# Kernel optimization log

Measured on AMD Instinct MI355X. Metric: run time of the kernel, lower is better.

Reference implementation:

```python
import jax, jax.numpy as jnp
import numpy as np

WS = 2048            # window_size
STEP = WS // 2       # hop = window_size // 2
NC = WS // 2 + 1     # rfft coeffs
NB = 4               # n_blocks


def _hann():
    # periodic hann window (torch.hann_window default)
    return 0.5 - 0.5 * jnp.cos(2.0 * jnp.pi * jnp.arange(WS) / WS)


def _block(x, transfer, gain):
    # x: (b, 1, time); transfer: (NC,); gain: scalar
    b, ch, time = x.shape
    frames = time // STEP
    padded = jnp.pad(x, ((0, 0), (0, 0), (0, STEP)))
    idx = jnp.arange(frames)[:, None] * STEP + jnp.arange(WS)[None, :]
    windowed = padded[:, :, idx]                       # (b, ch, F, WS)
    spec = jnp.fft.rfft(windowed, axis=-1)             # (b, ch, F, NC) complex
    spec_t = jnp.moveaxis(spec, 2, 0)                  # (F, b, ch, NC)
    tc = transfer.astype(spec.dtype)

    # linear recurrence: out_i = transfer * (spec_i + out_{i-1})
    def step_fn(carry, s):
        out = (s + carry) * tc
        return out, out

    _, outs = jax.lax.scan(step_fn, jnp.zeros_like(spec_t[0]), spec_t)
    wins = jnp.fft.irfft(outs, n=WS, axis=-1) * _hann()  # (F, b, ch, WS)
    wins = jnp.moveaxis(wins, 0, 2)                      # (b, ch, F, WS)
    # overlap-add with hop = WS/2: split each frame into two halves
    first = wins[..., :STEP].reshape(b, ch, frames * STEP)
    second = wins[..., STEP:].reshape(b, ch, frames * STEP)
    samples = (jnp.pad(first, ((0, 0), (0, 0), (0, STEP)))
               + jnp.pad(second, ((0, 0), (0, 0), (STEP, 0))))
    return jnp.tanh(samples * gain)[..., :time]


def setup_inputs() -> dict:
    key = jax.random.key(0)
    k_x, k_b, k_s, k_g = jax.random.split(key, 4)
    x = jax.random.normal(k_x, (32, 1, 262144), dtype=jnp.float32)
    # init_transfer: sparse resonances * scaling * pitch^2
    resonances = (jax.random.uniform(k_b, (NB, NC)) < 0.01).astype(jnp.float32)
    scaling = jax.random.uniform(k_s, (NB, NC), minval=0.9, maxval=0.998)
    pitch = jnp.linspace(1.0, 0.0, NC) ** 2
    transfers = resonances * scaling * pitch[None, :]
    gains = jax.random.uniform(k_g, (NB,), minval=10.0, maxval=200.0)
    mixer = jnp.zeros((NB + 1,), dtype=jnp.float32)
    return {"x": x, "transfers": transfers, "gains": gains, "mixer": mixer}


def reference(x, transfers, gains, mixer):
    outputs = [x]
    inp = x
    for i in range(NB):
        inp = _block(inp, transfers[i], gains[i])
        outputs.append(inp)
    stacked = jnp.stack(outputs, axis=-1)          # (b, 1, time, NB+1)
    mixer_values = jax.nn.softmax(mixer)
    return jnp.sum(stacked * mixer_values, axis=-1)
```

## Files before the change

kernel.cpp:

```cpp
#include <hip/hip_runtime.h>
#include <math.h>
#include <stdint.h>

#define NB   4
#define NC   1025
#define WSZ  2048
#define STEP 1024
#define FRM  256
#define BAT  32
#define TT   262144
#define SEGS 4
#define KC   16
#define YPAD 68

#define RREV (1.0f / 2048.0f)

typedef float f2 __attribute__((ext_vector_type(2)));

__device__ __forceinline__ float tanh_fast(float z) {
    float e = __expf(2.0f * z);
    return 1.0f - 2.0f / (e + 1.0f);
}

__device__ __forceinline__ void cis_rev(int idx, float* c, float* s) {
    float rev = (float)(idx & 2047) * RREV;
    *c = __builtin_amdgcn_cosf(rev);
    *s = __builtin_amdgcn_sinf(rev);
}

__global__ __launch_bounds__(1024) void setup_kernel(
    const float* __restrict__ transfers, const float* __restrict__ mixer,
    int* __restrict__ counts, int* __restrict__ bins, float* __restrict__ tvals,
    float* __restrict__ wmix, float* __restrict__ hann, int kmax)
{
    int i = blockIdx.x, tid = threadIdx.x;
    __shared__ int wcnt[16], woff[16];
    if (i == 0) {
        float cc, ss; cis_rev(tid, &cc, &ss);
        hann[tid] = 0.5f - 0.5f * cc;
    }
    float tv = transfers[i * NC + tid];
    bool nz = (tv != 0.0f);
    unsigned long long mask = __ballot(nz);
    int lane = tid & 63, w = tid >> 6;
    int within = __popcll(mask & ((1ULL << lane) - 1ULL));
    if (lane == 0) wcnt[w] = __popcll(mask);
    __syncthreads();
    if (tid == 0) {
        int acc = 0;
        for (int q = 0; q < 16; ++q) { woff[q] = acc; acc += wcnt[q]; }
        float tvL = transfers[i * NC + 1024];
        if (tvL != 0.0f && acc < kmax) { bins[i * NC + acc] = 1024; tvals[i * NC + acc] = tvL; acc++; }
        counts[i] = (acc < kmax) ? acc : kmax;
        if (i == 0) {
            float m = mixer[0];
            for (int q = 1; q < 5; ++q) m = fmaxf(m, mixer[q]);
            float e[5], s = 0.f;
            for (int q = 0; q < 5; ++q) { e[q] = __expf(mixer[q] - m); s += e[q]; }
            for (int q = 0; q < 5; ++q) wmix[q] = e[q] / s;
        }
    }
    __syncthreads();
    if (nz) {
        int pos = woff[w] + within;
        if (pos < kmax) { bins[i * NC + pos] = tid; tvals[i * NC + pos] = tv; }
    }
}

__global__ __launch_bounds__(256) void table_kernel(
    const int* __restrict__ counts, const int* __restrict__ bins,
    float2* __restrict__ cisA, float2* __restrict__ cisB, int kmax)
{
    int i = blockIdx.x >> 2, c = blockIdx.x & 3;
    int K = counts[i];
    int tid = threadIdx.x;
    for (int j = c; j < K; j += 4) {
        int k = bins[i * NC + j];
        if (tid < 64) {
            float cc, ss; cis_rev(k * tid, &cc, &ss);
            cisA[((size_t)i * kmax + j) * 64 + tid] = make_float2(cc, ss);
        } else if (tid < 80) {
            int q = tid - 64;
            float cc, ss; cis_rev(k * 64 * q, &cc, &ss);
            cisB[((size_t)i * kmax + j) * 16 + q] = make_float2(cc, ss);
        }
    }
}

__device__ __forceinline__ void half_dft(
    const float xr[16], int K, const float2* __restrict__ cA,
    const float2* __restrict__ cB, float2* __restrict__ Hout, int lane, int w)
{
    for (int j = w; j < K; j += 8) {
        int j2 = j + 4;
        bool two = (j2 < K);
        float2 bA = cB[(size_t)j * 16 + 1];
        float2 bB = two ? cB[(size_t)j2 * 16 + 1] : bA;
        float2 wAl = cA[(size_t)j * 64 + lane];
        float2 wBl = two ? cA[(size_t)j2 * 64 + lane] : wAl;
        f2 Wr, Wi, nWi;
        Wr.x = bA.x; Wr.y = bB.x;
        Wi.x = -bA.y; Wi.y = -bB.y;
        nWi = -Wi;
        f2 hr = 0.f, hi = 0.f;
#pragma unroll
        for (int i = 15; i >= 0; --i) {
            f2 xx; xx.x = xr[i]; xx.y = xr[i];
            f2 tmp = nWi * hi + xx;
            f2 nr = Wr * hr + tmp;
            hi = Wi * hr + Wr * hi;
            hr = nr;
        }
        f2 wlc, wls;
        wlc.x = wAl.x; wlc.y = wBl.x;
        wls.x = wAl.y; wls.y = wBl.y;
        f2 re = hr * wlc + hi * wls;
        f2 im = hi * wlc - hr * wls;
        float reA = re.x, imA = im.x, reB = re.y, imB = im.y;
#pragma unroll
        for (int m = 32; m >= 1; m >>= 1) {
            reA += __shfl_xor(reA, m, 64);
            imA += __shfl_xor(imA, m, 64);
            reB += __shfl_xor(reB, m, 64);
            imB += __shfl_xor(imB, m, 64);
        }
        if (lane == 0) {
            Hout[j] = make_float2(reA, imA);
            if (two) Hout[j2] = make_float2(reB, imB);
        }
    }
}

__global__ __launch_bounds__(256, 8) void analysis_kernel(
    const float* __restrict__ x, const int* __restrict__ counts,
    const float2* __restrict__ cisA, const float2* __restrict__ cisB,
    float2* __restrict__ H, int iblk, int kmax)
{
    int wg = blockIdx.x;
    int b = wg >> 8, h = wg & 255;
    int tid = threadIdx.x;
    int lane = tid & 63, w = tid >> 6;
    int K = counts[iblk];
    const float* xb = x + (size_t)b * TT + (size_t)h * STEP;
    float xr[16];
#pragma unroll
    for (int i = 0; i < 16; ++i) xr[i] = xb[lane + (i << 6)];
    const float2* cA = cisA + (size_t)iblk * kmax * 64;
    const float2* cB = cisB + (size_t)iblk * kmax * 16;
    float2* Hout = H + (size_t)(b * FRM + h) * K;
    half_dft(xr, K, cA, cB, Hout, lane, w);
}

__global__ __launch_bounds__(256) void scan_kernel(
    float2* __restrict__ S, const int* __restrict__ counts,
    const int* __restrict__ bins, const float* __restrict__ tvals, int iblk)
{
    int K = counts[iblk];
    int gw = (blockIdx.x << 2) + (threadIdx.x >> 6);
    int lane = threadIdx.x & 63;
    int b = gw & (BAT - 1), j0 = gw >> 5;
    for (int j = j0; j < K; j += 32) {
        float t = tvals[iblk * NC + j];
        int k = bins[iblk * NC + j];
        float sgn = (k & 1) ? -t : t;
        float2* Sb = S + (size_t)b * FRM * K + j;
        int f0 = lane << 2;
        float2 h1_0 = Sb[(size_t)(f0 + 0) * K];
        float2 h1_1 = Sb[(size_t)(f0 + 1) * K];
        float2 h1_2 = Sb[(size_t)(f0 + 2) * K];
        float2 h1_3 = Sb[(size_t)(f0 + 3) * K];
        float2 h1_4 = (f0 + 4 < FRM) ? Sb[(size_t)(f0 + 4) * K] : make_float2(0.f, 0.f);
        float ax0 = fmaf(sgn, h1_1.x, h1_0.x * t), ay0 = fmaf(sgn, h1_1.y, h1_0.y * t);
        float ax1 = fmaf(sgn, h1_2.x, h1_1.x * t), ay1 = fmaf(sgn, h1_2.y, h1_1.y * t);
        float ax2 = fmaf(sgn, h1_3.x, h1_2.x * t), ay2 = fmaf(sgn, h1_3.y, h1_2.y * t);
        float ax3 = fmaf(sgn, h1_4.x, h1_3.x * t), ay3 = fmaf(sgn, h1_4.y, h1_3.y * t);
        float Ax0 = ax0,                  Ay0 = ay0;
        float Ax1 = fmaf(t, Ax0, ax1),    Ay1 = fmaf(t, Ay0, ay1);
        float Ax2 = fmaf(t, Ax1, ax2),    Ay2 = fmaf(t, Ay1, ay2);
        float Ax3 = fmaf(t, Ax2, ax3),    Ay3 = fmaf(t, Ay2, ay3);
        float t2 = t * t, t4 = t2 * t2;
        float Px = Ax3, Py = Ay3;
        float w = t4;
#pragma unroll
        for (int d = 1; d <= 32; d <<= 1) {
            float ux = __shfl_up(Px, d, 64);
            float uy = __shfl_up(Py, d, 64);
            if (lane >= d) { Px = fmaf(w, ux, Px); Py = fmaf(w, uy, Py); }
            w *= w;
        }
        float Cx = __shfl_up(Px, 1, 64);
        float Cy = __shfl_up(Py, 1, 64);
        if (lane == 0) { Cx = 0.f; Cy = 0.f; }
        float t3 = t2 * t;
        Sb[(size_t)(f0 + 0) * K] = make_float2(fmaf(t,  Cx, Ax0), fmaf(t,  Cy, Ay0));
        Sb[(size_t)(f0 + 1) * K] = make_float2(fmaf(t2, Cx, Ax1), fmaf(t2, Cy, Ay1));
        Sb[(size_t)(f0 + 2) * K] = make_float2(fmaf(t3, Cx, Ax2), fmaf(t3, Cy, Ay2));
        Sb[(size_t)(f0 + 3) * K] = make_float2(fmaf(t4, Cx, Ax3), fmaf(t4, Cy, Ay3));
    }
}

__device__ __forceinline__ void acc4(
    f2& q0, f2& q1, f2& q2, f2& q3, float4 e, float4 a0, float4 a1)
{
    f2 up; up.x = e.x; up.y = e.y;
    f2 vp; vp.x = e.z; vp.y = e.w;
    q0 = up * a0.x + q0; q0 = vp * a0.y + q0;
    q1 = up * a0.z + q1; q1 = vp * a0.w + q1;
    q2 = up * a1.x + q2; q2 = vp * a1.y + q2;
    q3 = up * a1.z + q3; q3 = vp * a1.w + q3;
}

__global__ __launch_bounds__(256, 5) void fused_synth_kernel(
    const float2* __restrict__ S, float2* __restrict__ H2,
    const float2* __restrict__ cisA, const float2* __restrict__ cisB,
    const int* __restrict__ counts, const int* __restrict__ bins,
    const float* __restrict__ gains, const float* __restrict__ wmix,
    const float* __restrict__ hann, const float* __restrict__ x,
    float* __restrict__ dout, int iblk, int do_an, int kmax)
{
    __shared__ float4 smem[1216];
    float4* rc = smem;
    float*  ystage = (float*)smem;
    float4* part = smem + 1088;

    int wg = blockIdx.x;
    int b = wg >> 6, s0 = (wg & 63) << 2;
    int tid = threadIdx.x;
    int n1 = tid << 2;
    int q = tid >> 4;
    int m = (tid & 15) << 2;

    int K = counts[iblk];
    const int* bl = bins + iblk * NC;
    const float2* Ob = S + (size_t)b * FRM * K;
    const float2* cA0 = cisA + (size_t)iblk * kmax * 64;
    const float2* cB0 = cisB + (size_t)iblk * kmax * 16;

    f2 p00 = 0.f, p01 = 0.f, p02 = 0.f, p03 = 0.f;
    f2 p10 = 0.f, p11 = 0.f, p12 = 0.f, p13 = 0.f;
    f2 p20 = 0.f, p21 = 0.f, p22 = 0.f, p23 = 0.f;
    f2 p30 = 0.f, p31 = 0.f, p32 = 0.f, p33 = 0.f;

    for (int c0 = 0; c0 < K; c0 += KC) {
        int cs = (K - c0 < KC) ? (K - c0) : KC;
        {
            int flat = tid >> 2;
            int seg = flat >> 4;
            int j = flat & 15;
            int jj = c0 + ((j < cs) ? j : (cs - 1));
            int q0 = (tid & 3) << 2;
            int k = bl[jj];
            float g = ((k == 0) || (k == 1024)) ? (1.0f / 2048.0f) : (2.0f / 2048.0f);
            float sg = (k & 1) ? -g : g;
            int fc = s0 + seg;
            float2 o1 = Ob[(size_t)fc * K + jj];
            float2 om = (fc > 0) ? Ob[(size_t)(fc - 1) * K + jj] : make_float2(0.f, 0.f);
            float c2r = om.x * sg, c2i = om.y * sg;
            f2 u; u.x = c2r;  u.y = o1.x * g - c2r;
            f2 v; v.x = -c2i; v.y = -(o1.y * g - c2i);
            const float2* bqp = cB0 + (size_t)jj * 16 + q0;
#pragma unroll
            for (int e = 0; e < 4; ++e) {
                float2 bq = bqp[e];
                f2 up = u * bq.x + v * bq.y;
                f2 vp = v * bq.x - u * bq.y;
                rc[(flat << 4) + q0 + e] = make_float4(up.x, up.y, vp.x, vp.y);
            }
        }
        __syncthreads();
        const float2* cAj = cA0 + ((size_t)c0 << 6) + m;
        const float4* rcq = rc + q;
        int jj = 0;
        for (; jj + 2 <= cs; jj += 2) {
            float4 a00 = *(const float4*)(cAj);
            float4 a01 = *(const float4*)(cAj + 2);
            float4 a10 = *(const float4*)(cAj + 64);
            float4 a11 = *(const float4*)(cAj + 66);
            cAj += 128;
            {
                float4 e0 = rcq[(0 * KC + jj) << 4];
                float4 e1 = rcq[(0 * KC + jj + 1) << 4];
                acc4(p00, p01, p02, p03, e0, a00, a01);
                acc4(p00, p01, p02, p03, e1, a10, a11);
            }
            {
                float4 e0 = rcq[(1 * KC + jj) << 4];
                float4 e1 = rcq[(1 * KC + jj + 1) << 4];
                acc4(p10, p11, p12, p13, e0, a00, a01);
                acc4(p10, p11, p12, p13, e1, a10, a11);
            }
            {
                float4 e0 = rcq[(2 * KC + jj) << 4];
                float4 e1 = rcq[(2 * KC + jj + 1) << 4];
                acc4(p20, p21, p22, p23, e0, a00, a01);
                acc4(p20, p21, p22, p23, e1, a10, a11);
            }
            {
                float4 e0 = rcq[(3 * KC + jj) << 4];
                float4 e1 = rcq[(3 * KC + jj + 1) << 4];
                acc4(p30, p31, p32, p33, e0, a00, a01);
                acc4(p30, p31, p32, p33, e1, a10, a11);
            }
        }
        if (jj < cs) {
            float4 a0 = *(const float4*)(cAj);
            float4 a1 = *(const float4*)(cAj + 2);
            float4 e0 = rcq[(0 * KC + jj) << 4];
            float4 e1 = rcq[(1 * KC + jj) << 4];
            float4 e2 = rcq[(2 * KC + jj) << 4];
            float4 e3 = rcq[(3 * KC + jj) << 4];
            acc4(p00, p01, p02, p03, e0, a0, a1);
            acc4(p10, p11, p12, p13, e1, a0, a1);
            acc4(p20, p21, p22, p23, e2, a0, a1);
            acc4(p30, p31, p32, p33, e3, a0, a1);
        }
        __syncthreads();
    }

    size_t base0 = (size_t)b * TT + ((size_t)s0 << 10) + (size_t)n1;
    const float* prevsrc = (iblk == 0) ? x : dout;
    float4 hv = *(const float4*)(hann + n1);
    float gain = gains[iblk];
    float wsel = (iblk == 0) ? wmix[0] : 1.0f;
    float wn = wmix[iblk + 1];
    int cw = n1 >> 6, off = n1 & 63;

#define SEG_EPI(s, A0, A1, A2, A3)                                              \
    {                                                                           \
        float4 pv = *(const float4*)(prevsrc + base0 + ((size_t)(s) << 10));    \
        float4 yv;                                                              \
        yv.x = tanh_fast(fmaf(hv.x, A0.y, A0.x) * gain);                        \
        yv.y = tanh_fast(fmaf(hv.y, A1.y, A1.x) * gain);                        \
        yv.z = tanh_fast(fmaf(hv.z, A2.y, A2.x) * gain);                        \
        yv.w = tanh_fast(fmaf(hv.w, A3.y, A3.x) * gain);                        \
        float4 dv;                                                              \
        dv.x = fmaf(wsel, pv.x, wn * yv.x);                                     \
        dv.y = fmaf(wsel, pv.y, wn * yv.y);                                     \
        dv.z = fmaf(wsel, pv.z, wn * yv.z);                                     \
        dv.w = fmaf(wsel, pv.w, wn * yv.w);                                     \
        *(float4*)(dout + base0 + ((size_t)(s) << 10)) = dv;                    \
        if (do_an) *(float4*)(ystage + (s) * 16 * YPAD + cw * YPAD + off) = yv; \
    }

    SEG_EPI(0, p00, p01, p02, p03)
    SEG_EPI(1, p10, p11, p12, p13)
    SEG_EPI(2, p20, p21, p22, p23)
    SEG_EPI(3, p30, p31, p32, p33)
#undef SEG_EPI

    if (do_an) {
        __syncthreads();
        int K2 = counts[iblk + 1];
        if (K2 > 0) {
            const float2* cA2 = cisA + (size_t)(iblk + 1) * kmax * 64;
            const float2* cB2 = cisB + (size_t)(iblk + 1) * kmax * 16;
            int jloc = tid & 15, c = tid >> 4;
            int lane = tid & 63, wv = tid >> 6;
            const float4* yp0 = (const float4*)(ystage + c * YPAD);
            const float4* yp1 = (const float4*)(ystage + 16 * YPAD + c * YPAD);
            const float4* yp2 = (const float4*)(ystage + 32 * YPAD + c * YPAD);
            const float4* yp3 = (const float4*)(ystage + 48 * YPAD + c * YPAD);
            for (int jb = 0; jb < K2; jb += 16) {
                int j = jb + jloc;
                int js = (j < K2) ? j : (K2 - 1);
                float2 w1 = cA2[(size_t)js * 64 + 1];
                float Wr = w1.x, Wi = -w1.y, nWi = w1.y;
                f2 hrA = 0.f, hiA = 0.f;
                f2 hrB = 0.f, hiB = 0.f;
#pragma unroll
                for (int i4 = 15; i4 >= 0; --i4) {
                    float4 ya = yp0[i4];
                    float4 yb = yp1[i4];
                    float4 yc = yp2[i4];
                    float4 yd = yp3[i4];
#define HSTEP(CC)                                                                   \
                    { f2 yy; yy.x = ya.CC; yy.y = yb.CC;                            \
                      f2 t = hiA * nWi + yy; f2 nr = hrA * Wr + t;                  \
                      hiA = hrA * Wi + hiA * Wr; hrA = nr; }                        \
                    { f2 yy; yy.x = yc.CC; yy.y = yd.CC;                            \
                      f2 t = hiB * nWi + yy; f2 nr = hrB * Wr + t;                  \
                      hiB = hrB * Wi + hiB * Wr; hrB = nr; }
                    HSTEP(w)
                    HSTEP(z)
                    HSTEP(y)
                    HSTEP(x)
#undef HSTEP
                }
                float2 bq = cB2[(size_t)js * 16 + c];
                f2 reA = hrA * bq.x + hiA * bq.y;
                f2 imA = hiA * bq.x - hrA * bq.y;
                f2 reB = hrB * bq.x + hiB * bq.y;
                f2 imB = hiB * bq.x - hrB * bq.y;
                float4 prA = make_float4(reA.x, imA.x, reA.y, imA.y);
                float4 prB = make_float4(reB.x, imB.x, reB.y, imB.y);
#pragma unroll
                for (int d = 16; d <= 32; d <<= 1) {
                    prA.x += __shfl_xor(prA.x, d, 64);
                    prA.y += __shfl_xor(prA.y, d, 64);
                    prA.z += __shfl_xor(prA.z, d, 64);
                    prA.w += __shfl_xor(prA.w, d, 64);
                    prB.x += __shfl_xor(prB.x, d, 64);
                    prB.y += __shfl_xor(prB.y, d, 64);
                    prB.z += __shfl_xor(prB.z, d, 64);
                    prB.w += __shfl_xor(prB.w, d, 64);
                }
                if (lane < 16) {
                    part[wv * 16 + lane] = prA;
                    part[64 + wv * 16 + lane] = prB;
                }
                __syncthreads();
                if (tid < 32) {
                    int sel = tid >> 4, t = tid & 15;
                    int j2 = jb + t;
                    if (j2 < K2) {
                        const float4* pp = part + sel * 64;
                        float4 a0 = pp[t];
                        float4 a1 = pp[16 + t];
                        float4 a2 = pp[32 + t];
                        float4 a3 = pp[48 + t];
                        float4 acc;
                        acc.x = (a0.x + a1.x) + (a2.x + a3.x);
                        acc.y = (a0.y + a1.y) + (a2.y + a3.y);
                        acc.z = (a0.z + a1.z) + (a2.z + a3.z);
                        acc.w = (a0.w + a1.w) + (a2.w + a3.w);
                        H2[(size_t)(b * FRM + s0 + sel * 2) * K2 + j2] = make_float2(acc.x, acc.y);
                        H2[(size_t)(b * FRM + s0 + sel * 2 + 1) * K2 + j2] = make_float2(acc.z, acc.w);
                    }
                }
                __syncthreads();
            }
        }
    }
}

extern "C" void kernel_launch(void* const* d_in, const int* in_sizes, int n_in,
                              void* d_out, int out_size, void* d_ws, size_t ws_size,
                              hipStream_t stream)
{
    const float* x         = (const float*)d_in[0];
    const float* transfers = (const float*)d_in[1];
    const float* gains     = (const float*)d_in[2];
    const float* mixer     = (const float*)d_in[3];
    float* dout = (float*)d_out;

    uint8_t* ws = (uint8_t*)d_ws;
    int*   counts = (int*)ws;
    int*   bins   = (int*)(ws + 64);
    float* tvals  = (float*)(ws + 64 + 16400);
    float* wmix   = (float*)(ws + 64 + 16400 + 16400);
    float* hann   = (float*)(ws + 36864);
    const size_t HDR = 65536;

    long long perk = 2LL * BAT * FRM * 8 + (long long)NB * 80 * 8;
    long long km = ((long long)ws_size - (long long)HDR) / perk;
    int kmax = (int)((km < 1) ? 1 : ((km > NC) ? NC : km));
    float2* S0 = (float2*)(ws + HDR);
    float2* S1 = S0 + (size_t)BAT * FRM * kmax;
    float2* cisA = S1 + (size_t)BAT * FRM * kmax;
    float2* cisB = cisA + (size_t)NB * kmax * 64;

    setup_kernel<<<NB, 1024, 0, stream>>>(transfers, mixer, counts, bins, tvals, wmix, hann, kmax);
    table_kernel<<<NB * 4, 256, 0, stream>>>(counts, bins, cisA, cisB, kmax);
    analysis_kernel<<<BAT * FRM, 256, 0, stream>>>(x, counts, cisA, cisB, S0, 0, kmax);

    float2* cur = S0;
    float2* nxt = S1;
    for (int i = 0; i < NB; ++i) {
        scan_kernel<<<BAT * 8, 256, 0, stream>>>(cur, counts, bins, tvals, i);
        fused_synth_kernel<<<BAT * (FRM / SEGS), 256, 0, stream>>>(cur, nxt, cisA, cisB, counts, bins,
                                                                   gains, wmix, hann, x, dout, i,
                                                                   (i < NB - 1) ? 1 : 0, kmax);
        float2* t = cur; cur = nxt; nxt = t;
    }
}
```

Before: 235.9 us.

## Fuse recurrence scan into synthesis kernel and fold table build into setup

The separate scan kernel is removed. Each synthesis workgroup now recomputes the per-bin linear recurrence with a wavefront shuffle scan over frames up to its own segment, then stages only the few frames it needs in shared memory via readlane. The cis-table construction is also folded into the setup kernel. Together these drop several kernel launches and a global read-modify-write of the spectrum per block. The cost is redundant scan work in every workgroup, about half the frames on average, plus extra shared-memory syncs per chunk.

```diff
diff --git a/kernel.cpp b/kernel.cpp
--- a/kernel.cpp
+++ b/kernel.cpp
@@ -28,13 +28,19 @@
     *s = __builtin_amdgcn_sinf(rev);
 }
 
+__device__ __forceinline__ float rl(float v, int l) {
+    return __int_as_float(__builtin_amdgcn_readlane(__float_as_int(v), l));
+}
+
 __global__ __launch_bounds__(1024) void setup_kernel(
     const float* __restrict__ transfers, const float* __restrict__ mixer,
     int* __restrict__ counts, int* __restrict__ bins, float* __restrict__ tvals,
-    float* __restrict__ wmix, float* __restrict__ hann, int kmax)
+    float* __restrict__ wmix, float* __restrict__ hann,
+    float2* __restrict__ cisA, float2* __restrict__ cisB, int kmax)
 {
     int i = blockIdx.x, tid = threadIdx.x;
     __shared__ int wcnt[16], woff[16];
+    __shared__ int sK;
     if (i == 0) {
         float cc, ss; cis_rev(tid, &cc, &ss);
         hann[tid] = 0.5f - 0.5f * cc;
@@ -51,7 +57,9 @@
         for (int q = 0; q < 16; ++q) { woff[q] = acc; acc += wcnt[q]; }
         float tvL = transfers[i * NC + 1024];
         if (tvL != 0.0f && acc < kmax) { bins[i * NC + acc] = 1024; tvals[i * NC + acc] = tvL; acc++; }
-        counts[i] = (acc < kmax) ? acc : kmax;
+        int kk = (acc < kmax) ? acc : kmax;
+        counts[i] = kk;
+        sK = kk;
         if (i == 0) {
             float m = mixer[0];
             for (int q = 1; q < 5; ++q) m = fmaxf(m, mixer[q]);
@@ -65,22 +73,16 @@
         int pos = woff[w] + within;
         if (pos < kmax) { bins[i * NC + pos] = tid; tvals[i * NC + pos] = tv; }
     }
-}
-
-__global__ __launch_bounds__(256) void table_kernel(
-    const int* __restrict__ counts, const int* __restrict__ bins,
-    float2* __restrict__ cisA, float2* __restrict__ cisB, int kmax)
-{
-    int i = blockIdx.x >> 2, c = blockIdx.x & 3;
-    int K = counts[i];
-    int tid = threadIdx.x;
-    for (int j = c; j < K; j += 4) {
+    __syncthreads();
+    int K = sK;
+    for (int flat = tid; flat < K * 80; flat += 1024) {
+        int j = flat / 80, r = flat - j * 80;
         int k = bins[i * NC + j];
-        if (tid < 64) {
-            float cc, ss; cis_rev(k * tid, &cc, &ss);
-            cisA[((size_t)i * kmax + j) * 64 + tid] = make_float2(cc, ss);
-        } else if (tid < 80) {
-            int q = tid - 64;
+        if (r < 64) {
+            float cc, ss; cis_rev(k * r, &cc, &ss);
+            cisA[((size_t)i * kmax + j) * 64 + r] = make_float2(cc, ss);
+        } else {
+            int q = r - 64;
             float cc, ss; cis_rev(k * 64 * q, &cc, &ss);
             cisB[((size_t)i * kmax + j) * 16 + q] = make_float2(cc, ss);
         }
@@ -151,54 +153,6 @@
     half_dft(xr, K, cA, cB, Hout, lane, w);
 }
 
-__global__ __launch_bounds__(256) void scan_kernel(
-    float2* __restrict__ S, const int* __restrict__ counts,
-    const int* __restrict__ bins, const float* __restrict__ tvals, int iblk)
-{
-    int K = counts[iblk];
-    int gw = (blockIdx.x << 2) + (threadIdx.x >> 6);
-    int lane = threadIdx.x & 63;
-    int b = gw & (BAT - 1), j0 = gw >> 5;
-    for (int j = j0; j < K; j += 32) {
-        float t = tvals[iblk * NC + j];
-        int k = bins[iblk * NC + j];
-        float sgn = (k & 1) ? -t : t;
-        float2* Sb = S + (size_t)b * FRM * K + j;
-        int f0 = lane << 2;
-        float2 h1_0 = Sb[(size_t)(f0 + 0) * K];
-        float2 h1_1 = Sb[(size_t)(f0 + 1) * K];
-        float2 h1_2 = Sb[(size_t)(f0 + 2) * K];
-        float2 h1_3 = Sb[(size_t)(f0 + 3) * K];
-        float2 h1_4 = (f0 + 4 < FRM) ? Sb[(size_t)(f0 + 4) * K] : make_float2(0.f, 0.f);
-        float ax0 = fmaf(sgn, h1_1.x, h1_0.x * t), ay0 = fmaf(sgn, h1_1.y, h1_0.y * t);
-        float ax1 = fmaf(sgn, h1_2.x, h1_1.x * t), ay1 = fmaf(sgn, h1_2.y, h1_1.y * t);
-        float ax2 = fmaf(sgn, h1_3.x, h1_2.x * t), ay2 = fmaf(sgn, h1_3.y, h1_2.y * t);
-        float ax3 = fmaf(sgn, h1_4.x, h1_3.x * t), ay3 = fmaf(sgn, h1_4.y, h1_3.y * t);
-        float Ax0 = ax0,                  Ay0 = ay0;
-        float Ax1 = fmaf(t, Ax0, ax1),    Ay1 = fmaf(t, Ay0, ay1);
-        float Ax2 = fmaf(t, Ax1, ax2),    Ay2 = fmaf(t, Ay1, ay2);
-        float Ax3 = fmaf(t, Ax2, ax3),    Ay3 = fmaf(t, Ay2, ay3);
-        float t2 = t * t, t4 = t2 * t2;
-        float Px = Ax3, Py = Ay3;
-        float w = t4;
-#pragma unroll
-        for (int d = 1; d <= 32; d <<= 1) {
-            float ux = __shfl_up(Px, d, 64);
-            float uy = __shfl_up(Py, d, 64);
-            if (lane >= d) { Px = fmaf(w, ux, Px); Py = fmaf(w, uy, Py); }
-            w *= w;
-        }
-        float Cx = __shfl_up(Px, 1, 64);
-        float Cy = __shfl_up(Py, 1, 64);
-        if (lane == 0) { Cx = 0.f; Cy = 0.f; }
-        float t3 = t2 * t;
-        Sb[(size_t)(f0 + 0) * K] = make_float2(fmaf(t,  Cx, Ax0), fmaf(t,  Cy, Ay0));
-        Sb[(size_t)(f0 + 1) * K] = make_float2(fmaf(t2, Cx, Ax1), fmaf(t2, Cy, Ay1));
-        Sb[(size_t)(f0 + 2) * K] = make_float2(fmaf(t3, Cx, Ax2), fmaf(t3, Cy, Ay2));
-        Sb[(size_t)(f0 + 3) * K] = make_float2(fmaf(t4, Cx, Ax3), fmaf(t4, Cy, Ay3));
-    }
-}
-
 __device__ __forceinline__ void acc4(
     f2& q0, f2& q1, f2& q2, f2& q3, float4 e, float4 a0, float4 a1)
 {
@@ -211,17 +165,19 @@
 }
 
 __global__ __launch_bounds__(256, 5) void fused_synth_kernel(
-    const float2* __restrict__ S, float2* __restrict__ H2,
+    const float2* __restrict__ H, float2* __restrict__ H2,
     const float2* __restrict__ cisA, const float2* __restrict__ cisB,
     const int* __restrict__ counts, const int* __restrict__ bins,
-    const float* __restrict__ gains, const float* __restrict__ wmix,
-    const float* __restrict__ hann, const float* __restrict__ x,
-    float* __restrict__ dout, int iblk, int do_an, int kmax)
+    const float* __restrict__ tvals, const float* __restrict__ gains,
+    const float* __restrict__ wmix, const float* __restrict__ hann,
+    const float* __restrict__ x, float* __restrict__ dout,
+    int iblk, int do_an, int kmax)
 {
     __shared__ float4 smem[1216];
     float4* rc = smem;
     float*  ystage = (float*)smem;
     float4* part = smem + 1088;
+    float2* Olds = (float2*)(smem + 1088);
 
     int wg = blockIdx.x;
     int b = wg >> 6, s0 = (wg & 63) << 2;
@@ -232,7 +188,8 @@
 
     int K = counts[iblk];
     const int* bl = bins + iblk * NC;
-    const float2* Ob = S + (size_t)b * FRM * K;
+    const float* tv_ = tvals + iblk * NC;
+    const float2* Hb0 = H + (size_t)b * FRM * K;
     const float2* cA0 = cisA + (size_t)iblk * kmax * 64;
     const float2* cB0 = cisB + (size_t)iblk * kmax * 16;
 
@@ -243,6 +200,68 @@
 
     for (int c0 = 0; c0 < K; c0 += KC) {
         int cs = (K - c0 < KC) ? (K - c0) : KC;
+        {
+            int wv = tid >> 6, lane = tid & 63;
+            int mi = s0 >> 2;
+            int fmax = s0 + 4;
+            int f0 = lane << 2;
+#pragma unroll
+            for (int i5 = 0; i5 < 4; ++i5) {
+                int sl = wv + (i5 << 2);
+                int jj = c0 + ((sl < cs) ? sl : (cs - 1));
+                float t = tv_[jj];
+                int k = bl[jj];
+                float sgn = (k & 1) ? -t : t;
+                const float2* Hj = Hb0 + jj;
+                float2 z2 = make_float2(0.f, 0.f);
+                float2 h0 = (f0     <= fmax) ? Hj[(size_t)(f0    ) * K] : z2;
+                float2 h1 = (f0 + 1 <= fmax) ? Hj[(size_t)(f0 + 1) * K] : z2;
+                float2 h2 = (f0 + 2 <= fmax) ? Hj[(size_t)(f0 + 2) * K] : z2;
+                float2 h3 = (f0 + 3 <= fmax) ? Hj[(size_t)(f0 + 3) * K] : z2;
+                float h4x = __shfl_down(h0.x, 1, 64);
+                float h4y = __shfl_down(h0.y, 1, 64);
+                if (lane == 63) { h4x = 0.f; h4y = 0.f; }
+                float ax0 = fmaf(sgn, h1.x, h0.x * t), ay0 = fmaf(sgn, h1.y, h0.y * t);
+                float ax1 = fmaf(sgn, h2.x, h1.x * t), ay1 = fmaf(sgn, h2.y, h1.y * t);
+                float ax2 = fmaf(sgn, h3.x, h2.x * t), ay2 = fmaf(sgn, h3.y, h2.y * t);
+                float ax3 = fmaf(sgn, h4x,  h3.x * t), ay3 = fmaf(sgn, h4y,  h3.y * t);
+                float Ax0 = ax0,               Ay0 = ay0;
+                float Ax1 = fmaf(t, Ax0, ax1), Ay1 = fmaf(t, Ay0, ay1);
+                float Ax2 = fmaf(t, Ax1, ax2), Ay2 = fmaf(t, Ay1, ay2);
+                float Ax3 = fmaf(t, Ax2, ax3), Ay3 = fmaf(t, Ay2, ay3);
+                float t2 = t * t, t4 = t2 * t2, t3 = t2 * t;
+                float Px = Ax3, Py = Ay3;
+                float ww = t4;
+#pragma unroll
+                for (int d = 1; d <= 32; d <<= 1) {
+                    float ux = __shfl_up(Px, d, 64);
+                    float uy = __shfl_up(Py, d, 64);
+                    if (lane >= d) { Px = fmaf(ww, ux, Px); Py = fmaf(ww, uy, Py); }
+                    ww *= ww;
+                }
+                float Cx = __shfl_up(Px, 1, 64);
+                float Cy = __shfl_up(Py, 1, 64);
+                if (lane == 0) { Cx = 0.f; Cy = 0.f; }
+                float Ox0 = fmaf(t,  Cx, Ax0), Oy0 = fmaf(t,  Cy, Ay0);
+                float Ox1 = fmaf(t2, Cx, Ax1), Oy1 = fmaf(t2, Cy, Ay1);
+                float Ox2 = fmaf(t3, Cx, Ax2), Oy2 = fmaf(t3, Cy, Ay2);
+                float Ox3 = fmaf(t4, Cx, Ax3), Oy3 = fmaf(t4, Cy, Ay3);
+                float Omx = (s0 > 0) ? rl(Ox3, mi - 1) : 0.f;
+                float Omy = (s0 > 0) ? rl(Oy3, mi - 1) : 0.f;
+                float E0x = rl(Ox0, mi), E0y = rl(Oy0, mi);
+                float E1x = rl(Ox1, mi), E1y = rl(Oy1, mi);
+                float E2x = rl(Ox2, mi), E2y = rl(Oy2, mi);
+                float E3x = rl(Ox3, mi), E3y = rl(Oy3, mi);
+                if (lane == 0) {
+                    Olds[sl * 5 + 0] = make_float2(Omx, Omy);
+                    Olds[sl * 5 + 1] = make_float2(E0x, E0y);
+                    Olds[sl * 5 + 2] = make_float2(E1x, E1y);
+                    Olds[sl * 5 + 3] = make_float2(E2x, E2y);
+                    Olds[sl * 5 + 4] = make_float2(E3x, E3y);
+                }
+            }
+        }
+        __syncthreads();
         {
             int flat = tid >> 2;
             int seg = flat >> 4;
@@ -252,9 +271,8 @@
             int k = bl[jj];
             float g = ((k == 0) || (k == 1024)) ? (1.0f / 2048.0f) : (2.0f / 2048.0f);
             float sg = (k & 1) ? -g : g;
-            int fc = s0 + seg;
-            float2 o1 = Ob[(size_t)fc * K + jj];
-            float2 om = (fc > 0) ? Ob[(size_t)(fc - 1) * K + jj] : make_float2(0.f, 0.f);
+            float2 o1 = Olds[j * 5 + 1 + seg];
+            float2 om = Olds[j * 5 + seg];
             float c2r = om.x * sg, c2i = om.y * sg;
             f2 u; u.x = c2r;  u.y = o1.x * g - c2r;
             f2 v; v.x = -c2i; v.y = -(o1.y * g - c2i);
@@ -459,16 +477,16 @@
     float2* cisA = S1 + (size_t)BAT * FRM * kmax;
     float2* cisB = cisA + (size_t)NB * kmax * 64;
 
-    setup_kernel<<<NB, 1024, 0, stream>>>(transfers, mixer, counts, bins, tvals, wmix, hann, kmax);
-    table_kernel<<<NB * 4, 256, 0, stream>>>(counts, bins, cisA, cisB, kmax);
+    setup_kernel<<<NB, 1024, 0, stream>>>(transfers, mixer, counts, bins, tvals, wmix, hann,
+                                          cisA, cisB, kmax);
     analysis_kernel<<<BAT * FRM, 256, 0, stream>>>(x, counts, cisA, cisB, S0, 0, kmax);
 
     float2* cur = S0;
     float2* nxt = S1;
     for (int i = 0; i < NB; ++i) {
-        scan_kernel<<<BAT * 8, 256, 0, stream>>>(cur, counts, bins, tvals, i);
-        fused_synth_kernel<<<BAT * (FRM / SEGS), 256, 0, stream>>>(cur, nxt, cisA, cisB, counts, bins,
-                                                                   gains, wmix, hann, x, dout, i,
+        fused_synth_kernel<<<BAT * (FRM / SEGS), 256, 0, stream>>>(cur, nxt, cisA, cisB, counts,
+                                                                   bins, tvals, gains, wmix, hann,
+                                                                   x, dout, i,
                                                                    (i < NB - 1) ? 1 : 0, kmax);
         float2* t = cur; cur = nxt; nxt = t;
     }
```

After: 295.4 us. 1.25x slower.
